# Optimization experiments

Measured on AMD Instinct MI355X. Metric: run time of the kernel, lower is better.

Reference implementation:

```python
import jax, jax.numpy as jnp
import numpy as np

B, N, C, K = 8, 4096, 128, 20  # batch, points-per-cloud, channels (n_cout), knn neighbors
NEG_SLOPE = 0.01  # torch F.leaky_relu default


def setup_inputs() -> dict:
    key = jax.random.key(0)
    ks = jax.random.split(key, 6)
    s = 1.0 / np.sqrt(C).astype(np.float32)
    xyz = jax.random.normal(ks[0], (B, 3, N), jnp.float32)
    points = jax.random.normal(ks[1], (B, C, N), jnp.float32)
    Wc = jax.random.normal(ks[2], (C, C), jnp.float32) * s  # center 1x1 conv weight (out,in)
    bc = jax.random.normal(ks[3], (C,), jnp.float32) * s
    Wg = jax.random.normal(ks[4], (C, C), jnp.float32) * s  # grouped 1x1 conv weight
    bg = jax.random.normal(ks[5], (C,), jnp.float32) * s
    return {"xyz": xyz, "points": points, "Wc": Wc, "bc": bc, "Wg": Wg, "bg": bg}


def reference(xyz, points, Wc, bc, Wg, bg):
    # xyz: [B,3,N], points: [B,C,N]
    k = K
    shortcut = points
    p = jax.nn.leaky_relu(points, NEG_SLOPE)        # [B,C,N]
    pt = jnp.transpose(p, (0, 2, 1))                # [B,N,C]
    xt = jnp.transpose(xyz, (0, 2, 1))              # [B,N,3]

    # pairwise squared distances [B,N,N]
    sq_norm = jnp.sum(xt * xt, axis=-1)             # [B,N]
    sq = sq_norm[:, :, None] - 2.0 * jnp.einsum('bnd,bmd->bnm', xt, xt) + sq_norm[:, None, :]

    # knn: k+1 nearest (incl. self), drop self -> [B,N,k]
    _, idx = jax.lax.top_k(-sq, k + 1)
    idx = idx[:, :, 1:]

    # gather neighbor features: [B,N,k,C]
    grouped = jax.vmap(lambda a, i: a[i])(pt, idx)

    # center 1x1 conv on [B,C,1,N] == per-point linear
    center = jnp.einsum('oc,bcn->bon', Wc, p) + bc[None, :, None]      # [B,C,N]
    # grouped 1x1 conv on [B,C,k,N]
    gout = jnp.einsum('oc,bnkc->bokn', Wg, grouped) + bg[None, :, None, None]  # [B,C,k,N]

    # mean over concat([center(1), grouped(k)], axis=2) then residual
    pooled = (center + jnp.sum(gout, axis=2)) / (k + 1)
    return pooled + shortcut
```

## Files before the change

### kernel.cpp

```cpp
#include <hip/hip_runtime.h>

#define B 8
#define N 4096
#define C 128
#define C2 256
#define KNN 21
#define CAP 22

typedef unsigned long long u64;
typedef unsigned int u32;
typedef unsigned short u16;

typedef __attribute__((ext_vector_type(8))) short bf16x8;
typedef __attribute__((ext_vector_type(4))) float f32x4;

__device__ __forceinline__ float bf2f(u16 u) {
    return __uint_as_float(((u32)u) << 16);
}
__device__ __forceinline__ u16 f2bf(float f) {
    u32 x = __float_as_uint(f);
    return (u16)((x + 0x7FFFu + ((x >> 16) & 1u)) >> 16);
}

__global__ __launch_bounds__(256) void k_transpose_lrelu(
        const float* __restrict__ pts, u16* __restrict__ X,
        const float* __restrict__ xyz, float4* __restrict__ cand) {
    __shared__ u16 tile[32][33];
    int b  = blockIdx.z;
    int c0 = blockIdx.y * 32;
    int n0 = blockIdx.x * 32;
    int tx = threadIdx.x, ty = threadIdx.y;

    if (blockIdx.y == 0 && ty == 0) {
        int n = n0 + tx;
        const float* xz = xyz + (size_t)b * 3 * N;
        float x = xz[n], y = xz[N + n], z = xz[2 * N + n];
        float sn = __fadd_rn(__fadd_rn(__fmul_rn(x, x), __fmul_rn(y, y)),
                             __fmul_rn(z, z));
        cand[(size_t)b * N + n] = make_float4(x, y, z, sn);
    }

    const float* src = pts + (size_t)b * C * N;
    #pragma unroll
    for (int i = 0; i < 32; i += 8) {
        float v = src[(size_t)(c0 + ty + i) * N + n0 + tx];
        if (v < 0.f) v = __fmul_rn(v, 0.01f);
        tile[ty + i][tx] = f2bf(v);
    }
    __syncthreads();
    u16* dst = X + (size_t)b * N * C2;
    #pragma unroll
    for (int i = 0; i < 32; i += 8) {
        dst[(size_t)(n0 + ty + i) * C2 + (c0 + tx)] = tile[tx][ty + i];
    }
}

__global__ __launch_bounds__(256) void k_knn_gather(
        const float4* __restrict__ cand, u16* __restrict__ X) {
    __shared__ __align__(16) char lds[52224];
    float4* stg  = (float4*)lds;
    u32*    kbuf = (u32*)(lds + 18432);
    u16*    ibuf = (u16*)(lds + 18432 + 22528);
    u64*    mg   = (u64*)lds;
    __shared__ u16 win[64 * KNN];

    int tid = threadIdx.x;
    int w = tid >> 6, l = tid & 63;
    int b = blockIdx.y;
    int n0 = blockIdx.x * 64;
    int nq = n0 + l;

    const float4* candb = cand + (size_t)b * N;
    float4 cq = candb[nq];
    float qx = cq.x, qy = cq.y, qz = cq.z, snq = cq.w;

    u32 key[KNN], idx[KNN];
    #pragma unroll
    for (int i = 0; i < KNN; ++i) { key[i] = 0xFFFFFFFFu; idx[i] = 0u; }
    int cnt = 0;
    u32 thr = 0xFFFFFFFFu;

    auto compact = [&]() {
        #pragma unroll 1
        for (int i = 0; i < CAP; ++i) {
            if (__ballot(i < cnt) == 0ull) break;
            u32 kv = kbuf[i * 256 + tid];
            u32 iv = ibuf[i * 256 + tid];
            bool ins = (i < cnt) && (kv < key[20]);
            if (__ballot(ins) != 0ull) {
                key[20] = ins ? kv : key[20];
                idx[20] = ins ? iv : idx[20];
                #pragma unroll
                for (int t = 19; t >= 0; --t) {
                    bool sw = key[t] > key[t + 1];
                    if (__ballot(sw) == 0ull) break;
                    u32 ka = sw ? key[t + 1] : key[t];
                    u32 kz = sw ? key[t] : key[t + 1];
                    u32 ia = sw ? idx[t + 1] : idx[t];
                    u32 iz = sw ? idx[t] : idx[t + 1];
                    key[t] = ka; key[t + 1] = kz;
                    idx[t] = ia; idx[t + 1] = iz;
                }
            }
        }
        cnt = 0;
        thr = key[20];
    };

    float4* mystg = stg + w * 288;
    int wl = l + (l >> 3);

    for (int sc = 0; sc < 4; ++sc) {
        int m0 = w * 1024 + sc * 256;
        float4 v0 = candb[m0 + l];
        float4 v1 = candb[m0 + l + 64];
        float4 v2 = candb[m0 + l + 128];
        float4 v3 = candb[m0 + l + 192];
        mystg[wl]       = v0;
        mystg[wl + 72]  = v1;
        mystg[wl + 144] = v2;
        mystg[wl + 216] = v3;
        asm volatile("s_waitcnt lgkmcnt(0)" ::: "memory");
        for (int cc = 0; cc < 256; cc += 8) {
            int base = cc + (cc >> 3);
            #pragma unroll
            for (int j = 0; j < 8; ++j) {
                float4 cp = mystg[base + j];
                int m = m0 + cc + j;
                float dot = __fadd_rn(__fadd_rn(__fmul_rn(qx, cp.x),
                                                __fmul_rn(qy, cp.y)),
                                      __fmul_rn(qz, cp.z));
                float sq = __fadd_rn(__fsub_rn(snq, __fadd_rn(dot, dot)), cp.w);
                u32 bits = __float_as_uint(sq);
                u32 kb = bits ^ (0x80000000u | (u32)(((int)bits) >> 31));
                kbuf[cnt * 256 + tid] = kb;
                ibuf[cnt * 256 + tid] = (u16)m;
                cnt += (kb < thr);
            }
            if (__ballot(cnt >= 15) != 0ull) compact();
        }
    }
    compact();

    __syncthreads();
    #pragma unroll
    for (int j = 0; j < KNN; ++j)
        mg[(w * 64 + l) * KNN + j] = ((u64)key[j] << 32) | (u64)idx[j];
    __syncthreads();

    if (w == 0) {
        int p0 = 0, p1 = 0, p2 = 0, p3 = 0;
        for (int j = 0; j < KNN; ++j) {
            u64 c0 = mg[(0 * 64 + l) * KNN + p0];
            u64 c1 = mg[(1 * 64 + l) * KNN + p1];
            u64 c2 = mg[(2 * 64 + l) * KNN + p2];
            u64 c3 = mg[(3 * 64 + l) * KNN + p3];
            u64 m01 = c0 < c1 ? c0 : c1; int s01 = c0 < c1 ? 0 : 1;
            u64 m23 = c2 < c3 ? c2 : c3; int s23 = c2 < c3 ? 2 : 3;
            u64 mm = m01 < m23 ? m01 : m23;
            int sel = m01 < m23 ? s01 : s23;
            win[l * KNN + j] = (u16)(mm & 0xFFFFu);
            p0 += (sel == 0); p1 += (sel == 1); p2 += (sel == 2); p3 += (sel == 3);
        }
    }
    __syncthreads();

    const u16* Xb = X + (size_t)b * N * C2;
    for (int qq = 0; qq < 16; ++qq) {
        int q = w * 16 + qq;
        float f0 = 0.f, f1 = 0.f;
        #pragma unroll
        for (int j = 1; j < KNN; ++j) {
            int m = win[q * KNN + j];
            u32 u2 = *(const u32*)(Xb + (size_t)m * C2 + 2 * l);
            f0 += bf2f((u16)(u2 & 0xFFFFu));
            f1 += bf2f((u16)(u2 >> 16));
        }
        u16* dst = X + ((size_t)b * N + n0 + q) * C2 + 128 + 2 * l;
        *(u32*)dst = ((u32)f2bf(f1) << 16) | (u32)f2bf(f0);
    }
}

__global__ __launch_bounds__(256) void k_gemm_mfma(
        const u16* __restrict__ X, const float* __restrict__ Wc,
        const float* __restrict__ Wg, const float* __restrict__ pts,
        const float* __restrict__ bc, const float* __restrict__ bg,
        float* __restrict__ out) {
    __shared__ u16 xs[64][264];
    int bid = blockIdx.x;
    int b  = bid >> 6;
    int n0 = (bid & 63) * 64;
    int tid = threadIdx.x;

    const u16* Xb = X + (size_t)b * N * C2;
    #pragma unroll
    for (int it = 0; it < 8; ++it) {
        int t = it * 256 + tid;
        int r = t >> 5, cch = t & 31;
        *(bf16x8*)(&xs[r][cch * 8]) =
            *(const bf16x8*)(Xb + (size_t)(n0 + r) * C2 + cch * 8);
    }
    __syncthreads();

    int w = tid >> 6, lane = tid & 63;
    int l16 = lane & 15, lq = lane >> 4;
    const float* wc0 = Wc + (size_t)(w * 32 + l16) * 128 + lq * 8;
    const float* wc1 = Wc + (size_t)(w * 32 + 16 + l16) * 128 + lq * 8;
    const float* wg0 = Wg + (size_t)(w * 32 + l16) * 128 + lq * 8;
    const float* wg1 = Wg + (size_t)(w * 32 + 16 + l16) * 128 + lq * 8;

    f32x4 acc[2][4];
    #pragma unroll
    for (int oo = 0; oo < 2; ++oo)
        #pragma unroll
        for (int t = 0; t < 4; ++t)
            acc[oo][t] = (f32x4){0.f, 0.f, 0.f, 0.f};

    #pragma unroll
    for (int kk = 0; kk < 8; ++kk) {
        const float* s0 = (kk < 4) ? (wc0 + kk * 32) : (wg0 + (kk - 4) * 32);
        const float* s1 = (kk < 4) ? (wc1 + kk * 32) : (wg1 + (kk - 4) * 32);
        float4 wa0 = *(const float4*)s0, wb0 = *(const float4*)(s0 + 4);
        float4 wa1 = *(const float4*)s1, wb1 = *(const float4*)(s1 + 4);
        bf16x8 a0, a1;
        a0[0] = (short)f2bf(wa0.x); a0[1] = (short)f2bf(wa0.y);
        a0[2] = (short)f2bf(wa0.z); a0[3] = (short)f2bf(wa0.w);
        a0[4] = (short)f2bf(wb0.x); a0[5] = (short)f2bf(wb0.y);
        a0[6] = (short)f2bf(wb0.z); a0[7] = (short)f2bf(wb0.w);
        a1[0] = (short)f2bf(wa1.x); a1[1] = (short)f2bf(wa1.y);
        a1[2] = (short)f2bf(wa1.z); a1[3] = (short)f2bf(wa1.w);
        a1[4] = (short)f2bf(wb1.x); a1[5] = (short)f2bf(wb1.y);
        a1[6] = (short)f2bf(wb1.z); a1[7] = (short)f2bf(wb1.w);
        #pragma unroll
        for (int t = 0; t < 4; ++t) {
            bf16x8 bt = *(const bf16x8*)(&xs[t * 16 + l16][lq * 8 + kk * 32]);
            acc[0][t] = __builtin_amdgcn_mfma_f32_16x16x32_bf16(a0, bt,
                                                                acc[0][t], 0, 0, 0);
            acc[1][t] = __builtin_amdgcn_mfma_f32_16x16x32_bf16(a1, bt,
                                                                acc[1][t], 0, 0, 0);
        }
    }

    const float inv21 = 1.0f / 21.0f;
    const float* pb = pts + (size_t)b * C * N;
    float* ob = out + (size_t)b * C * N;
    #pragma unroll
    for (int oo = 0; oo < 2; ++oo) {
        float bias[4];
        #pragma unroll
        for (int r = 0; r < 4; ++r) {
            int o = w * 32 + oo * 16 + lq * 4 + r;
            bias[r] = bc[o] + 20.f * bg[o];
        }
        #pragma unroll
        for (int t = 0; t < 4; ++t) {
            int n = n0 + t * 16 + l16;
            #pragma unroll
            for (int r = 0; r < 4; ++r) {
                int o = w * 32 + oo * 16 + lq * 4 + r;
                ob[(size_t)o * N + n] =
                    (acc[oo][t][r] + bias[r]) * inv21 + pb[(size_t)o * N + n];
            }
        }
    }
}

extern "C" void kernel_launch(void* const* d_in, const int* in_sizes, int n_in,
                              void* d_out, int out_size, void* d_ws, size_t ws_size,
                              hipStream_t stream) {
    const float* xyz = (const float*)d_in[0];
    const float* pts = (const float*)d_in[1];
    const float* Wc  = (const float*)d_in[2];
    const float* bc  = (const float*)d_in[3];
    const float* Wg  = (const float*)d_in[4];
    const float* bg  = (const float*)d_in[5];
    float* out = (float*)d_out;

    u16* X = (u16*)d_ws;
    float4* cand = (float4*)((char*)d_ws +
                             (size_t)B * N * C2 * sizeof(u16));

    k_transpose_lrelu<<<dim3(N / 32, C / 32, B), dim3(32, 8), 0, stream>>>(
        pts, X, xyz, cand);
    k_knn_gather<<<dim3(N / 64, B), dim3(256), 0, stream>>>(cand, X);
    k_gemm_mfma<<<dim3(512), dim3(256), 0, stream>>>(X, Wc, Wg, pts, bc, bg, out);
}
```

Before: 311.4 us.

## Fuse kNN gather with MFMA GEMM and shrink intermediate buffer to C channels

Merges the kNN/gather kernel with the GEMM kernel so the summed neighbour features go straight into LDS next to the center features, instead of being written to a 256-wide global buffer and reloaded. The workspace row width drops from 256 to 128, which removes one kernel launch and the global round-trip. It also drops the early-exit ballot in the insertion bubble, making that loop branch-free at the cost of always doing all swaps. The fused kernel reuses the kNN LDS region for the GEMM tile and raises per-block register pressure.

Result: faster. 267.9 us (-14.0%).

```diff
diff --git a/kernel.cpp b/kernel.cpp
--- a/kernel.cpp
+++ b/kernel.cpp
@@ -3,7 +3,7 @@
 #define B 8
 #define N 4096
 #define C 128
-#define C2 256
+#define CL 128
 #define KNN 21
 #define CAP 22
 
@@ -48,20 +48,24 @@
         tile[ty + i][tx] = f2bf(v);
     }
     __syncthreads();
-    u16* dst = X + (size_t)b * N * C2;
+    u16* dst = X + (size_t)b * N * CL;
     #pragma unroll
     for (int i = 0; i < 32; i += 8) {
-        dst[(size_t)(n0 + ty + i) * C2 + (c0 + tx)] = tile[tx][ty + i];
-    }
-}
-
-__global__ __launch_bounds__(256) void k_knn_gather(
-        const float4* __restrict__ cand, u16* __restrict__ X) {
+        dst[(size_t)(n0 + ty + i) * CL + (c0 + tx)] = tile[tx][ty + i];
+    }
+}
+
+__global__ __launch_bounds__(256) void k_knn_gemm(
+        const float4* __restrict__ cand, const u16* __restrict__ X,
+        const float* __restrict__ Wc, const float* __restrict__ Wg,
+        const float* __restrict__ pts, const float* __restrict__ bc,
+        const float* __restrict__ bg, float* __restrict__ out) {
     __shared__ __align__(16) char lds[52224];
     float4* stg  = (float4*)lds;
     u32*    kbuf = (u32*)(lds + 18432);
     u16*    ibuf = (u16*)(lds + 18432 + 22528);
     u64*    mg   = (u64*)lds;
+    u16 (*xs)[264] = (u16(*)[264])lds;
     __shared__ u16 win[64 * KNN];
 
     int tid = threadIdx.x;
@@ -93,7 +97,6 @@
                 #pragma unroll
                 for (int t = 19; t >= 0; --t) {
                     bool sw = key[t] > key[t + 1];
-                    if (__ballot(sw) == 0ull) break;
                     u32 ka = sw ? key[t + 1] : key[t];
                     u32 kz = sw ? key[t] : key[t + 1];
                     u32 ia = sw ? idx[t + 1] : idx[t];
@@ -165,44 +168,30 @@
     }
     __syncthreads();
 
-    const u16* Xb = X + (size_t)b * N * C2;
+    const u16* Xb = X + (size_t)b * N * CL;
+    #pragma unroll
+    for (int it = 0; it < 4; ++it) {
+        int t = it * 256 + tid;
+        int r = t >> 4, cch = t & 15;
+        *(bf16x8*)(&xs[r][cch * 8]) =
+            *(const bf16x8*)(Xb + (size_t)(n0 + r) * CL + cch * 8);
+    }
     for (int qq = 0; qq < 16; ++qq) {
         int q = w * 16 + qq;
         float f0 = 0.f, f1 = 0.f;
         #pragma unroll
         for (int j = 1; j < KNN; ++j) {
             int m = win[q * KNN + j];
-            u32 u2 = *(const u32*)(Xb + (size_t)m * C2 + 2 * l);
+            u32 u2 = *(const u32*)(Xb + (size_t)m * CL + 2 * l);
             f0 += bf2f((u16)(u2 & 0xFFFFu));
             f1 += bf2f((u16)(u2 >> 16));
         }
-        u16* dst = X + ((size_t)b * N + n0 + q) * C2 + 128 + 2 * l;
-        *(u32*)dst = ((u32)f2bf(f1) << 16) | (u32)f2bf(f0);
-    }
-}
-
-__global__ __launch_bounds__(256) void k_gemm_mfma(
-        const u16* __restrict__ X, const float* __restrict__ Wc,
-        const float* __restrict__ Wg, const float* __restrict__ pts,
-        const float* __restrict__ bc, const float* __restrict__ bg,
-        float* __restrict__ out) {
-    __shared__ u16 xs[64][264];
-    int bid = blockIdx.x;
-    int b  = bid >> 6;
-    int n0 = (bid & 63) * 64;
-    int tid = threadIdx.x;
-
-    const u16* Xb = X + (size_t)b * N * C2;
-    #pragma unroll
-    for (int it = 0; it < 8; ++it) {
-        int t = it * 256 + tid;
-        int r = t >> 5, cch = t & 31;
-        *(bf16x8*)(&xs[r][cch * 8]) =
-            *(const bf16x8*)(Xb + (size_t)(n0 + r) * C2 + cch * 8);
-    }
-    __syncthreads();
-
-    int w = tid >> 6, lane = tid & 63;
+        *(u32*)(&xs[q][128 + 2 * l]) =
+            ((u32)f2bf(f1) << 16) | (u32)f2bf(f0);
+    }
+    __syncthreads();
+
+    int lane = tid & 63;
     int l16 = lane & 15, lq = lane >> 4;
     const float* wc0 = Wc + (size_t)(w * 32 + l16) * 128 + lq * 8;
     const float* wc1 = Wc + (size_t)(w * 32 + 16 + l16) * 128 + lq * 8;
@@ -278,10 +267,10 @@
 
     u16* X = (u16*)d_ws;
     float4* cand = (float4*)((char*)d_ws +
-                             (size_t)B * N * C2 * sizeof(u16));
+                             (size_t)B * N * CL * sizeof(u16));
 
     k_transpose_lrelu<<<dim3(N / 32, C / 32, B), dim3(32, 8), 0, stream>>>(
         pts, X, xyz, cand);
-    k_knn_gather<<<dim3(N / 64, B), dim3(256), 0, stream>>>(cand, X);
-    k_gemm_mfma<<<dim3(512), dim3(256), 0, stream>>>(X, Wc, Wg, pts, bc, bg, out);
-}
+    k_knn_gemm<<<dim3(N / 64, B), dim3(256), 0, stream>>>(
+        cand, X, Wc, Wg, pts, bc, bg, out);
+}
```
